# Kernel tuning notes

Measured on AMD Instinct MI355X. Metric: run time of the kernel, lower is better.

The kernel has to match this reference:

```python
import jax, jax.numpy as jnp
import numpy as np

SIZE, NC, BITS = 16, 3, 8
NV = NC * BITS * SIZE * SIZE  # 6144
NH = NV
N = 32
K_LS = 32   # fixed cap on T=0 local-search Gibbs sweeps (converged rows are fixed points)
K_CP = 16   # fixed cap on coupling MH iterations (converged rows masked out)


def float2bit(x, bits=BITS):
    # quantize [0,1) floats to `bits` binary planes, as in float2bit(...).flatten(1)
    q = jnp.clip(jnp.floor(x * (2 ** bits)), 0, 2 ** bits - 1).astype(jnp.int32)
    shifts = jnp.arange(bits, dtype=jnp.int32)
    b = (q[..., None] >> shifts) & 1  # [N,nc,H,W,bits]
    return b.astype(jnp.float32)


def energy(params, v, h0, h1):
    W0, W1, b0, b1, b2 = params
    e = -jnp.sum(v * b0, axis=1)
    e = e - jnp.sum(h0 * (v @ W0.T + b1), axis=1)
    e = e - jnp.sum(h1 * (h0 @ W1.T + b2), axis=1)
    return e


def _samp(logits, r, T):
    if T == 0:
        return (logits >= 0).astype(jnp.float32)
    return (r < jax.nn.sigmoid(logits / T)).astype(jnp.float32)


def gibbs_step(params, v, h0, h1, even, fix_v, T, key):
    W0, W1, b0, b1, b2 = params
    if T == 0:
        rv = rh0 = rh1 = None
    else:
        kv, k0, k1 = jax.random.split(key, 3)
        rv = jax.random.uniform(kv, v.shape)
        rh0 = jax.random.uniform(k0, h0.shape)
        rh1 = jax.random.uniform(k1, h1.shape)
    # 'even' sweep order: v -> odd h layers -> even h layers
    v_e = v if fix_v else _samp(h0 @ W0 + b0, rv, T)
    h1_e = _samp(h0 @ W1.T + b2, rh1, T)
    h0_e = _samp(v_e @ W0.T + b1 + h1_e @ W1, rh0, T)
    # 'odd' sweep order: even h layers -> v -> odd h layers
    h0_o = _samp(v @ W0.T + b1 + h1 @ W1, rh0, T)
    v_o = v if fix_v else _samp(h0_o @ W0 + b0, rv, T)
    h1_o = _samp(h0_o @ W1.T + b2, rh1, T)
    m = even[:, None]
    return (jnp.where(m, v_e, v_o), jnp.where(m, h0_e, h0_o), jnp.where(m, h1_e, h1_o))


def local_search(params, v, h0, h1, fix_v, key):
    # T=0 deterministic descent with a fixed per-row even/odd split (rand_u drawn once);
    # converged rows are fixed points of the map, so running a fixed K_LS sweeps over the
    # full batch is equivalent to the torch masked while-loop (up to the iteration cap).
    even = jax.random.uniform(key, (v.shape[0],)) < 0.5
    def body(i, s):
        return gibbs_step(params, s[0], s[1], s[2], even, fix_v, 0, None)
    return jax.lax.fori_loop(0, K_LS, body, (v, h0, h1))


def mh_step(params, v, h0, h1, fix_v, key):
    kv, k0, k1, ku = jax.random.split(key, 4)
    v_p = v if fix_v else (jax.random.uniform(kv, v.shape) < 0.5).astype(jnp.float32)
    h0_p = (jax.random.uniform(k0, h0.shape) < 0.5).astype(jnp.float32)
    h1_p = (jax.random.uniform(k1, h1.shape) < 0.5).astype(jnp.float32)
    log_ratio = energy(params, v, h0, h1) - energy(params, v_p, h0_p, h1_p)
    acc = jax.random.uniform(ku, (v.shape[0],)) < jnp.exp(jnp.minimum(log_ratio, 0.0))
    a = acc[:, None]
    return (v if fix_v else jnp.where(a, v_p, v), jnp.where(a, h0_p, h0), jnp.where(a, h1_p, h1))


def _conv_mask(v_new, h0_new, h1_new, v, h0, h1, fix_v):
    c = jnp.ones(v.shape[0], bool) if fix_v else jnp.all(v_new == v, axis=1)
    return c & jnp.all(h0_new == h0, axis=1) & jnp.all(h1_new == h1, axis=1)


def coupling(params, v, h0, h1, fix_v, key):
    k0, key = jax.random.split(key)
    v1, h01, h11 = mh_step(params, v, h0, h1, fix_v, k0)
    e = energy(params, v1, h01, h11)
    conv = _conv_mask(v1, h01, h11, v, h0, h1, fix_v)
    def body(state, k):
        v, h0, h1, e, conv = state
        v2, h02, h12 = mh_step(params, v, h0, h1, fix_v, k)
        de = energy(params, v2, h02, h12) - energy(params, v, h0, h1)
        m = ~conv
        e = e + jnp.where(m, de, 0.0)
        conv2 = _conv_mask(v2, h02, h12, v, h0, h1, fix_v)
        mm = m[:, None]
        v = jnp.where(mm, v2, v)
        h0 = jnp.where(mm, h02, h0)
        h1 = jnp.where(mm, h12, h1)
        return (v, h0, h1, e, conv | conv2), None
    keys = jax.random.split(key, K_CP)
    (v, h0, h1, e, conv), _ = jax.lax.scan(body, (v1, h01, h11, e, conv), keys)
    return e, v, h0, h1


def _dbm_loss(v_img, W0, W1, b0, b1, b2):
    params = (W0, W1, b0, b1, b2)
    n = v_img.shape[0]
    ks = jax.random.split(jax.random.key(42), 13)
    v = float2bit(v_img).reshape(n, -1)
    # positive phase (visibles clamped, fix_v=True)
    h0 = (jax.random.uniform(ks[0], (n, NH)) < 0.5).astype(jnp.float32)
    h1 = (jax.random.uniform(ks[1], (n, NH)) < 0.5).astype(jnp.float32)
    v, h0, h1 = local_search(params, v, h0, h1, True, ks[2])
    even = jax.random.uniform(ks[3], (n,)) < 0.5
    v, h0, h1 = gibbs_step(params, v, h0, h1, even, True, 1, ks[4])
    e_pos, v, h0, h1 = coupling(params, v, h0, h1, True, ks[5])
    # negative phase (free-running)
    v = (jax.random.uniform(ks[6], v.shape) < 0.5).astype(jnp.float32)
    h0 = (jax.random.uniform(ks[7], (n, NH)) < 0.5).astype(jnp.float32)
    h1 = (jax.random.uniform(ks[8], (n, NH)) < 0.5).astype(jnp.float32)
    v, h0, h1 = local_search(params, v, h0, h1, False, ks[9])
    even = jax.random.uniform(ks[10], (n,)) < 0.5
    v, h0, h1 = gibbs_step(params, v, h0, h1, even, False, 1, ks[11])
    e_neg, v, h0, h1 = coupling(params, v, h0, h1, False, ks[12])
    return e_pos - e_neg  # [N]


def setup_inputs() -> dict:
    key = jax.random.key(0)
    kv, kw0, kw1 = jax.random.split(key, 3)
    v = jax.random.uniform(kv, (N, NC, SIZE, SIZE), dtype=jnp.float32)
    # orthogonal-like scale (unit-norm rows): entries ~ 1/sqrt(fan_in)
    W0 = jax.random.normal(kw0, (NH, NV), dtype=jnp.float32) / np.sqrt(NV)
    W1 = jax.random.normal(kw1, (NH, NH), dtype=jnp.float32) / np.sqrt(NH)
    b0 = jnp.zeros((NV,), jnp.float32)
    b1 = jnp.zeros((NH,), jnp.float32)
    b2 = jnp.zeros((NH,), jnp.float32)
    return {"v": v, "W0": W0, "W1": W1, "b0": b0, "b1": b1, "b2": b2}


def reference(v, W0, W1, b0, b1, b2):
    return _dbm_loss(v, W0, W1, b0, b1, b2)
```

## Files before the change

kernel.cpp:

```cpp
#include <hip/hip_runtime.h>
#include <cstdint>
#include <math.h>

typedef unsigned int u32;
typedef unsigned long long u64;
typedef double d4 __attribute__((ext_vector_type(4)));

#define TF_PARTITIONABLE 1

#define NU 6144
#define NB 32
#define NTOT (NU * NB)
#define NWORD 96
#define NCH 16
#define CHK 384
#define NT_TILES 12
#define HALF_BIG 98304u
#define HALF_SMALL 16u

struct Key { u32 a, b; };
struct UVec { float u[NB]; };

__host__ __device__ __forceinline__ void tf2x32(u32 k0, u32 k1, u32 x0, u32 x1, u32& o0, u32& o1) {
  const u32 k2 = k0 ^ k1 ^ 0x1BD11BDAu;
#define TFR(r) { x0 += x1; x1 = (x1 << r) | (x1 >> (32 - r)); x1 ^= x0; }
  x0 += k0; x1 += k1;
  TFR(13) TFR(15) TFR(26) TFR(6)  x0 += k1; x1 += k2 + 1u;
  TFR(17) TFR(29) TFR(16) TFR(24) x0 += k2; x1 += k0 + 2u;
  TFR(13) TFR(15) TFR(26) TFR(6)  x0 += k0; x1 += k1 + 3u;
  TFR(17) TFR(29) TFR(16) TFR(24) x0 += k1; x1 += k2 + 4u;
  TFR(13) TFR(15) TFR(26) TFR(6)  x0 += k2; x1 += k0 + 5u;
#undef TFR
  o0 = x0; o1 = x1;
}

__host__ __device__ __forceinline__ u32 rbits(u32 k0, u32 k1, u32 t, u32 half) {
#if TF_PARTITIONABLE
  (void)half;
  u32 a, b; tf2x32(k0, k1, 0u, t, a, b); return a ^ b;
#else
  u32 a, b;
  if (t < half) { tf2x32(k0, k1, t, half + t, a, b); return a; }
  tf2x32(k0, k1, t - half, t, a, b); return b;
#endif
}

__host__ __device__ __forceinline__ float u01f(u32 bits) {
  union { u32 u; float f; } c; c.u = (bits >> 9) | 0x3f800000u;
  return c.f - 1.0f;
}

__device__ __forceinline__ double pav(int probe, int l) {
  return probe ? (double)(((l * 13 + 5) & 63) + 1) : (double)(l + 1);
}
__device__ __forceinline__ double pbv(int probe, int l) {
  return probe ? (double)(((l * 11 + 2) & 63) + 1) : (double)(((l * 7 + 3) & 63) + 1);
}

__global__ __launch_bounds__(64) void k_calib(int* __restrict__ tbl) {
  int L = threadIdx.x;
  d4 z = {0.0, 0.0, 0.0, 0.0};
  d4 o0 = __builtin_amdgcn_mfma_f64_16x16x4f64(pav(0, L), pbv(0, L), z, 0, 0, 0);
  d4 o1 = __builtin_amdgcn_mfma_f64_16x16x4f64(pav(1, L), pbv(1, L), z, 0, 0, 0);
  int q = L >> 4, m16 = L & 15;
  int best = -1;
  for (int combo = 0; combo < 16; ++combo) {
    int fa = combo & 1, fb = (combo >> 1) & 1, fd = combo >> 2;
    int ok = 1;
    for (int probe = 0; probe < 2; ++probe) {
#pragma unroll
      for (int r = 0; r < 4; ++r) {
        int i, j;
        if (fd == 0)      { j = m16; i = 4 * q + r; }
        else if (fd == 1) { j = m16; i = q + 4 * r; }
        else if (fd == 2) { i = m16; j = 4 * q + r; }
        else              { i = m16; j = q + 4 * r; }
        double pred = 0.0;
#pragma unroll
        for (int k = 0; k < 4; ++k) {
          int la = fa ? (i * 4 + k) : (k * 16 + i);
          int lb = fb ? (j * 4 + k) : (k * 16 + j);
          pred += pav(probe, la) * pbv(probe, lb);
        }
        double obs = probe ? (r == 0 ? o1[0] : r == 1 ? o1[1] : r == 2 ? o1[2] : o1[3])
                           : (r == 0 ? o0[0] : r == 1 ? o0[1] : r == 2 ? o0[2] : o0[3]);
        if (pred != obs) ok = 0;
      }
    }
    if (__all(ok) && best < 0) best = combo;
  }
  int mA = 0, kA = 0, nB = 0, kB = 0, b0_ = 0, bs = 0, j0 = 0, js = 0, okf = 0;
  if (best >= 0) {
    int fa = best & 1, fb = (best >> 1) & 1, fd = best >> 2;
    if (fa) { mA = L >> 2; kA = L & 3; } else { mA = m16; kA = q; }
    if (fb) { nB = L >> 2; kB = L & 3; } else { nB = m16; kB = q; }
    if (fd == 0)      { j0 = m16; js = 0; b0_ = 4 * q; bs = 1; }
    else if (fd == 1) { j0 = m16; js = 0; b0_ = q; bs = 4; }
    else if (fd == 2) { b0_ = m16; bs = 0; j0 = 4 * q; js = 1; }
    else              { b0_ = m16; bs = 0; j0 = q; js = 4; }
    okf = 1;
  }
  int* p = tbl + L * 16;
  p[0] = mA; p[1] = kA; p[2] = nB; p[3] = kB;
  p[4] = b0_; p[5] = bs; p[6] = j0; p[7] = js; p[8] = okf;
}

__global__ void k_init(u32* __restrict__ flag, u32* __restrict__ chg) { *flag = 0u; *chg = 0u; }

__global__ void k_conv(u32* __restrict__ flag, u32* __restrict__ chg) {
  if (*flag == 0u && *chg == 0u) *flag = 1u;
  *chg = 0u;
}

__global__ void k_allconv(const u32* __restrict__ conv, u32* __restrict__ skipc) {
  if (*skipc) return;
  u32 all = 1u;
  for (int b = 0; b < NB; ++b) all &= conv[b];
  if (all) *skipc = 1u;
}

__global__ __launch_bounds__(256) void k_pos_v(const float* __restrict__ vin, u64* __restrict__ pk) {
  int tid = blockIdx.x * 256 + threadIdx.x;
  int b = tid / 768, p = tid % 768;
  float x = vin[tid];
  int q = (int)floorf(x * 256.0f);
  q = q < 0 ? 0 : (q > 255 ? 255 : q);
  ((unsigned char*)pk)[b * 768 + p] = (unsigned char)q;
}

__global__ __launch_bounds__(256) void k_bern(u32 k0, u32 k1, u64* __restrict__ pk) {
  int tid = blockIdx.x * 256 + threadIdx.x;
  bool s = u01f(rbits(k0, k1, (u32)tid, HALF_BIG)) < 0.5f;
  u64 m = __ballot(s);
  if ((threadIdx.x & 63) == 0) pk[tid >> 6] = m;
}

__global__ __launch_bounds__(256) void k_bern3(u32 has_v, u32 va, u32 vb, u32 ha0, u32 hb0,
                                               u32 ha1, u32 hb1,
                                               u64* __restrict__ pkv, u64* __restrict__ pkh0,
                                               u64* __restrict__ pkh1, const u32* __restrict__ skip) {
  if (skip && *skip) return;
  int tid = blockIdx.x * 256 + threadIdx.x;
  int lane0 = (threadIdx.x & 63) == 0;
  if (has_v) {
    bool s = u01f(rbits(va, vb, (u32)tid, HALF_BIG)) < 0.5f;
    u64 m = __ballot(s);
    if (lane0) pkv[tid >> 6] = m;
  }
  { bool s = u01f(rbits(ha0, hb0, (u32)tid, HALF_BIG)) < 0.5f;
    u64 m = __ballot(s);
    if (lane0) pkh0[tid >> 6] = m; }
  { bool s = u01f(rbits(ha1, hb1, (u32)tid, HALF_BIG)) < 0.5f;
    u64 m = __ballot(s);
    if (lane0) pkh1[tid >> 6] = m; }
}

__device__ __forceinline__ bool samp_dec(float f, int t1, u32 k0, u32 k1, u32 tid) {
  if (t1) {
    double u = (double)u01f(rbits(k0, k1, tid, HALF_BIG));
    return u < 1.0 / (1.0 + exp(-(double)f));
  }
  return f >= 0.0f;
}

__global__ __launch_bounds__(256) void k_samp(const float* __restrict__ fE, const float* __restrict__ fO,
                                              u32 even, int t1, u32 k0, u32 k1,
                                              u64* __restrict__ pk,
                                              const u32* __restrict__ skip, u32* __restrict__ chg) {
  if (skip && *skip) return;
  int tid = blockIdx.x * 256 + threadIdx.x;
  int b = tid / NU;
  float f = ((even >> b) & 1u) ? fE[tid] : fO[tid];
  bool s = samp_dec(f, t1, k0, k1, (u32)tid);
  u64 m = __ballot(s);
  if ((threadIdx.x & 63) == 0) {
    int widx = tid >> 6;
    if (chg) { u64 old = pk[widx]; if (old != m) *chg = 1u; }
    pk[widx] = m;
  }
}

__global__ __launch_bounds__(256) void k_gemm_n(const float* __restrict__ W, const u64* __restrict__ pkx,
                                                double* __restrict__ part, const u32* __restrict__ skip,
                                                const int* __restrict__ tbl) {
  if (skip && *skip) return;
  __shared__ double smem_d[2560];
  int jt = blockIdx.x % 96, c = blockIdx.x / 96;
  int wid = threadIdx.x >> 6, lane = threadIdx.x & 63;
  int kbase = c * CHK;
  int jn0 = jt * 64;
  const int* tp = tbl + lane * 16;
  int okf = tp[8];
  if (okf) {
    float* lw = (float*)smem_d;
    int mA = tp[0], kA = tp[1], nB = tp[2], kB = tp[3];
    int bD0 = tp[4], bDs = tp[5], jD0 = tp[6], jDs = tp[7];
    int t256 = threadIdx.x;
    d4 acc0 = {0.0, 0.0, 0.0, 0.0};
    d4 acc1 = {0.0, 0.0, 0.0, 0.0};
#pragma unroll
    for (int r = 0; r < 2; ++r) {
      int idx = r * 256 + t256, kk = idx >> 4, qq = idx & 15;
      float4 w4 = *(const float4*)(W + (size_t)(kbase + kk) * NU + jn0 + 4 * qq);
      float* d = &lw[kk * 80 + 4 * qq];
      d[0] = w4.x; d[1] = w4.y; d[2] = w4.z; d[3] = w4.w;
    }
    __syncthreads();
    const u64* pxr0 = pkx + (size_t)mA * NWORD + (kbase >> 6);
    const u64* pxr1 = pkx + (size_t)(mA + 16) * NWORD + (kbase >> 6);
    int buf = 0;
    for (int t = 0; t < NT_TILES; ++t) {
      float4 w0p, w1p;
      bool pf = (t + 1) < NT_TILES;
      if (pf) {
        int k0n = kbase + (t + 1) * 32;
        { int idx = t256,       kk = idx >> 4, qq = idx & 15;
          w0p = *(const float4*)(W + (size_t)(k0n + kk) * NU + jn0 + 4 * qq); }
        { int idx = 256 + t256, kk = idx >> 4, qq = idx & 15;
          w1p = *(const float4*)(W + (size_t)(k0n + kk) * NU + jn0 + 4 * qq); }
      }
      u64 ww0 = pxr0[t >> 1], ww1 = pxr1[t >> 1];
      u32 sh = ((u32)(t & 1) << 5) + (u32)kA;
      u32 bb0 = (u32)(ww0 >> sh), bb1 = (u32)(ww1 >> sh);
      const float* lwp = &lw[(buf * 32 + kB) * 80 + wid * 16 + nB];
#pragma unroll
      for (int u = 0; u < 8; ++u) {
        double a0 = (double)((bb0 >> (4 * u)) & 1u);
        double a1 = (double)((bb1 >> (4 * u)) & 1u);
        double wv = (double)lwp[320 * u];
        acc0 = __builtin_amdgcn_mfma_f64_16x16x4f64(a0, wv, acc0, 0, 0, 0);
        acc1 = __builtin_amdgcn_mfma_f64_16x16x4f64(a1, wv, acc1, 0, 0, 0);
      }
      if (pf) {
        int nb = buf ^ 1;
        { int idx = t256,       kk = idx >> 4, qq = idx & 15;
          float* d = &lw[(nb * 32 + kk) * 80 + 4 * qq];
          d[0] = w0p.x; d[1] = w0p.y; d[2] = w0p.z; d[3] = w0p.w; }
        { int idx = 256 + t256, kk = idx >> 4, qq = idx & 15;
          float* d = &lw[(nb * 32 + kk) * 80 + 4 * qq];
          d[0] = w1p.x; d[1] = w1p.y; d[2] = w1p.z; d[3] = w1p.w; }
      }
      __syncthreads();
      buf ^= 1;
    }
    int jn = jn0 + wid * 16;
    double* pp = part + (size_t)c * NTOT + jn;
#pragma unroll
    for (int r = 0; r < 4; ++r) {
      int bi = bD0 + bDs * r, jj = jD0 + jDs * r;
      pp[(size_t)bi * NU + jj] = acc0[r];
      pp[(size_t)(bi + 16) * NU + jj] = acc1[r];
    }
  } else {
    double* red = smem_d;
    int j = jn0 + lane;
    int i0 = kbase + wid * (CHK / 4);
    const float* wp = W + (size_t)i0 * NU + j;
    double acc[32];
#pragma unroll
    for (int b = 0; b < 32; ++b) acc[b] = 0.0;
    for (int i = 0; i < CHK / 4; ++i) {
      double w = (double)wp[(size_t)i * NU];
      int k = i0 + i;
#pragma unroll
      for (int b = 0; b < 32; ++b) {
        double xb = (double)((pkx[(size_t)b * NWORD + (k >> 6)] >> (k & 63)) & 1ull);
        acc[b] = fma(xb, w, acc[b]);
      }
    }
    for (int w = 1; w < 4; ++w) {
      if (wid == w) {
#pragma unroll
        for (int b = 0; b < 32; ++b) red[b * 64 + lane] = acc[b];
      }
      __syncthreads();
      if (wid == 0) {
#pragma unroll
        for (int b = 0; b < 32; ++b) acc[b] += red[b * 64 + lane];
      }
      __syncthreads();
    }
    if (wid == 0) {
      double* pp = part + (size_t)c * NTOT + j;
#pragma unroll
      for (int b = 0; b < 32; ++b) pp[(size_t)b * NU] = acc[b];
    }
  }
}

__global__ __launch_bounds__(256) void k_gemm_t(const float* __restrict__ W, const u64* __restrict__ pkx,
                                                double* __restrict__ part, const u32* __restrict__ skip,
                                                const int* __restrict__ tbl) {
  if (skip && *skip) return;
  __shared__ double smem_d[2176];
  int jt = blockIdx.x % 96, c = blockIdx.x / 96;
  int wid = threadIdx.x >> 6, lane = threadIdx.x & 63;
  int kbase = c * CHK;
  int jn0 = jt * 64;
  const int* tp = tbl + lane * 16;
  int okf = tp[8];
  if (okf) {
    float* lw = (float*)smem_d;
    int mA = tp[0], kA = tp[1], nB = tp[2], kB = tp[3];
    int bD0 = tp[4], bDs = tp[5], jD0 = tp[6], jDs = tp[7];
    int t256 = threadIdx.x;
    d4 acc0 = {0.0, 0.0, 0.0, 0.0};
    d4 acc1 = {0.0, 0.0, 0.0, 0.0};
#pragma unroll
    for (int r = 0; r < 2; ++r) {
      int idx = r * 256 + t256, jj = idx >> 3, kq = idx & 7;
      float4 w4 = *(const float4*)(W + (size_t)(jn0 + jj) * NU + kbase + 4 * kq);
      float* d = &lw[jj * 34 + 4 * kq];
      d[0] = w4.x; d[1] = w4.y; d[2] = w4.z; d[3] = w4.w;
    }
    __syncthreads();
    const u64* pxr0 = pkx + (size_t)mA * NWORD + (kbase >> 6);
    const u64* pxr1 = pkx + (size_t)(mA + 16) * NWORD + (kbase >> 6);
    int buf = 0;
    for (int t = 0; t < NT_TILES; ++t) {
      float4 w0p, w1p;
      bool pf = (t + 1) < NT_TILES;
      if (pf) {
        int k0n = kbase + (t + 1) * 32;
        { int idx = t256,       jj = idx >> 3, kq = idx & 7;
          w0p = *(const float4*)(W + (size_t)(jn0 + jj) * NU + k0n + 4 * kq); }
        { int idx = 256 + t256, jj = idx >> 3, kq = idx & 7;
          w1p = *(const float4*)(W + (size_t)(jn0 + jj) * NU + k0n + 4 * kq); }
      }
      u64 ww0 = pxr0[t >> 1], ww1 = pxr1[t >> 1];
      u32 sh = ((u32)(t & 1) << 5) + (u32)kA;
      u32 bb0 = (u32)(ww0 >> sh), bb1 = (u32)(ww1 >> sh);
      const float* lwp = &lw[(buf * 64 + wid * 16 + nB) * 34 + kB];
#pragma unroll
      for (int u = 0; u < 8; ++u) {
        double a0 = (double)((bb0 >> (4 * u)) & 1u);
        double a1 = (double)((bb1 >> (4 * u)) & 1u);
        double wv = (double)lwp[4 * u];
        acc0 = __builtin_amdgcn_mfma_f64_16x16x4f64(a0, wv, acc0, 0, 0, 0);
        acc1 = __builtin_amdgcn_mfma_f64_16x16x4f64(a1, wv, acc1, 0, 0, 0);
      }
      if (pf) {
        int nb = buf ^ 1;
        { int idx = t256,       jj = idx >> 3, kq = idx & 7;
          float* d = &lw[(nb * 64 + jj) * 34 + 4 * kq];
          d[0] = w0p.x; d[1] = w0p.y; d[2] = w0p.z; d[3] = w0p.w; }
        { int idx = 256 + t256, jj = idx >> 3, kq = idx & 7;
          float* d = &lw[(nb * 64 + jj) * 34 + 4 * kq];
          d[0] = w1p.x; d[1] = w1p.y; d[2] = w1p.z; d[3] = w1p.w; }
      }
      __syncthreads();
      buf ^= 1;
    }
    int jn = jn0 + wid * 16;
    double* pp = part + (size_t)c * NTOT + jn;
#pragma unroll
    for (int r = 0; r < 4; ++r) {
      int bi = bD0 + bDs * r, jj = jD0 + jDs * r;
      pp[(size_t)bi * NU + jj] = acc0[r];
      pp[(size_t)(bi + 16) * NU + jj] = acc1[r];
    }
  } else {
    float* lwf = (float*)smem_d;
    double* red = smem_d;
    int qf = threadIdx.x & 7, af = threadIdx.x >> 3;
    double acc[32];
#pragma unroll
    for (int b = 0; b < 32; ++b) acc[b] = 0.0;
    for (int s = 0; s < NT_TILES; ++s) {
      int ib = kbase + s * 32;
#pragma unroll
      for (int pass = 0; pass < 2; ++pass) {
        int r = pass * 32 + af;
        float4 w4 = *(const float4*)(W + (size_t)(jn0 + r) * NU + ib + qf * 4);
        lwf[(qf * 4 + 0) * 65 + r] = w4.x;
        lwf[(qf * 4 + 1) * 65 + r] = w4.y;
        lwf[(qf * 4 + 2) * 65 + r] = w4.z;
        lwf[(qf * 4 + 3) * 65 + r] = w4.w;
      }
      __syncthreads();
      int iw = wid * 8;
      for (int ii = 0; ii < 8; ++ii) {
        double w = (double)lwf[(iw + ii) * 65 + lane];
        int k = ib + iw + ii;
#pragma unroll
        for (int b = 0; b < 32; ++b) {
          double xb = (double)((pkx[(size_t)b * NWORD + (k >> 6)] >> (k & 63)) & 1ull);
          acc[b] = fma(xb, w, acc[b]);
        }
      }
      __syncthreads();
    }
    for (int w = 1; w < 4; ++w) {
      if (wid == w) {
#pragma unroll
        for (int b = 0; b < 32; ++b) red[b * 64 + lane] = acc[b];
      }
      __syncthreads();
      if (wid == 0) {
#pragma unroll
        for (int b = 0; b < 32; ++b) acc[b] += red[b * 64 + lane];
      }
      __syncthreads();
    }
    if (wid == 0) {
      double* pp = part + (size_t)c * NTOT + jn0 + lane;
#pragma unroll
      for (int b = 0; b < 32; ++b) pp[(size_t)b * NU] = acc[b];
    }
  }
}

__global__ __launch_bounds__(256) void k_reduce(const double* __restrict__ part, const float* __restrict__ bias,
                                                const float* __restrict__ src, float* __restrict__ out,
                                                const u32* __restrict__ skip) {
  if (skip && *skip) return;
  int tid = blockIdx.x * 256 + threadIdx.x;
  int j = tid % NU;
  double s = src ? (double)src[tid] : 0.0;
  if (bias) s += (double)bias[j];
#pragma unroll
  for (int c = 0; c < NCH; ++c) s += part[(size_t)c * NTOT + tid];
  out[tid] = (float)s;
}

__global__ __launch_bounds__(256) void k_redsamp(const double* __restrict__ part, const float* __restrict__ bias,
                                                 const float* __restrict__ src, float* __restrict__ out,
                                                 int t1, u32 k0, u32 k1,
                                                 u64* __restrict__ pk,
                                                 const u32* __restrict__ skip, u32 wmask,
                                                 u32* __restrict__ chg) {
  if (skip && *skip) return;
  int tid = blockIdx.x * 256 + threadIdx.x;
  int j = tid % NU, b = tid / NU;
  double s = src ? (double)src[tid] : 0.0;
  if (bias) s += (double)bias[j];
#pragma unroll
  for (int c = 0; c < NCH; ++c) s += part[(size_t)c * NTOT + tid];
  float f = (float)s;
  if (out) out[tid] = f;
  bool wr = (wmask >> b) & 1u;
  bool smp = samp_dec(f, t1, k0, k1, (u32)tid);
  u64 m = __ballot(smp);
  if (((threadIdx.x & 63) == 0) && wr) {
    int widx = tid >> 6;
    if (chg) { u64 old = pk[widx]; if (old != m) *chg = 1u; }
    pk[widx] = m;
  }
  (void)j;
}

__global__ __launch_bounds__(256) void k_energy(const u64* __restrict__ pkv, const u64* __restrict__ pkh0,
                                                const u64* __restrict__ pkh1, const float* __restrict__ f1,
                                                const float* __restrict__ f2, const float* __restrict__ b0,
                                                float* __restrict__ eout, const u32* __restrict__ skip) {
  if (skip && *skip) return;
  __shared__ double red[256];
  int b = blockIdx.x, t = threadIdx.x;
  double s = 0.0;
  for (int j = t; j < NU; j += 256) {
    int w = j >> 6, bit = j & 63;
    if ((pkv [b * NWORD + w] >> bit) & 1ull) s += (double)b0[j];
    if ((pkh0[b * NWORD + w] >> bit) & 1ull) s += (double)f1[(size_t)b * NU + j];
    if ((pkh1[b * NWORD + w] >> bit) & 1ull) s += (double)f2[(size_t)b * NU + j];
  }
  red[t] = s; __syncthreads();
  for (int off = 128; off > 0; off >>= 1) { if (t < off) red[t] += red[t + off]; __syncthreads(); }
  if (t == 0) eout[b] = (float)(-red[0]);
}

__global__ __launch_bounds__(64) void k_accept(float* __restrict__ ecur, const float* __restrict__ eprop,
                                               float* __restrict__ erun, u32* __restrict__ conv,
                                               u32* __restrict__ accf,
                                               const u64* __restrict__ pv, const u64* __restrict__ pcv,
                                               const u64* __restrict__ ph0, const u64* __restrict__ pch0,
                                               const u64* __restrict__ ph1, const u64* __restrict__ pch1,
                                               UVec uv, int first, const u32* __restrict__ skip) {
  if (skip && *skip) return;
  int b = blockIdx.x, t = threadIdx.x;
  u64 diff = 0ull;
  for (int w = t; w < NWORD; w += 64) {
    size_t o = (size_t)b * NWORD + w;
    if (pv) diff |= pv[o] ^ pcv[o];
    diff |= ph0[o] ^ pch0[o];
    diff |= ph1[o] ^ pch1[o];
  }
  int neq = __any(diff != 0ull);
  if (t == 0) {
    float ec = ecur[b], ep = eprop[b];
    bool acc = (double)uv.u[b] < exp(fmin((double)ec - (double)ep, 0.0));
    bool m = first ? true : (conv[b] == 0u);
    bool upd = m && acc;
    if (first) erun[b] = acc ? ep : ec;
    else if (upd) erun[b] += (ep - ec);
    if (upd) ecur[b] = ep;
    u32 c2 = acc ? (neq ? 0u : 1u) : 1u;
    conv[b] = first ? c2 : (conv[b] | c2);
    accf[b] = upd ? 1u : 0u;
  }
}

__global__ __launch_bounds__(256) void k_merge_pk(const u32* __restrict__ accf,
                                                  const u64* __restrict__ pa, u64* __restrict__ ca,
                                                  const u64* __restrict__ pb, u64* __restrict__ cb,
                                                  const u64* __restrict__ pc, u64* __restrict__ cc,
                                                  const u32* __restrict__ skip) {
  if (skip && *skip) return;
  int w = blockIdx.x * 256 + threadIdx.x;
  if (w >= NB * NWORD) return;
  int b = w / NWORD;
  if (accf[b]) {
    ca[w] = pa[w];
    cb[w] = pb[w];
    if (pc) cc[w] = pc[w];
  }
}

__global__ void k_final(const float* __restrict__ ep, const float* __restrict__ en, float* __restrict__ out) {
  int b = threadIdx.x;
  if (b < NB) out[b] = ep[b] - en[b];
}

static void split_keys(Key k, int n, Key* out) {
#if TF_PARTITIONABLE
  for (int i = 0; i < n; ++i) { u32 a, b; tf2x32(k.a, k.b, 0u, (u32)i, a, b); out[i].a = a; out[i].b = b; }
#else
  u32 flat[64];
  for (int i = 0; i < n; ++i) { u32 a, b; tf2x32(k.a, k.b, (u32)i, (u32)(n + i), a, b); flat[i] = a; flat[n + i] = b; }
  for (int i = 0; i < n; ++i) { out[i].a = flat[2 * i]; out[i].b = flat[2 * i + 1]; }
#endif
}
static u32 mask32(Key k) {
  u32 m = 0;
  for (int b = 0; b < NB; ++b)
    if (u01f(rbits(k.a, k.b, (u32)b, HALF_SMALL)) < 0.5f) m |= (1u << b);
  return m;
}

extern "C" void kernel_launch(void* const* d_in, const int* in_sizes, int n_in,
                              void* d_out, int out_size, void* d_ws, size_t ws_size,
                              hipStream_t stream) {
  const float* vin = (const float*)d_in[0];
  const float* W0  = (const float*)d_in[1];
  const float* W1  = (const float*)d_in[2];
  const float* b0  = (const float*)d_in[3];
  const float* b1  = (const float*)d_in[4];
  const float* b2  = (const float*)d_in[5];
  float* outp = (float*)d_out;

  char* ws = (char*)d_ws;
  size_t off = 0;
  auto alloc = [&](size_t bytes) -> void* {
    void* p = ws + off; off += (bytes + 255) & ~(size_t)255; return p;
  };
  enum { SV = 0, SH0, SH1, SVE, SH1E, SH0O, SVP, SH0P, SH1P, NS };
  enum { IV = 0, IA, IB, IC, ID, IE, IF2, NF };
  u64* PK[NS]; float* F[NF];
  for (int f = 0; f < NF; ++f) F[f] = (float*)alloc((size_t)NTOT * 4);
  double* PART = (double*)alloc((size_t)NCH * NTOT * 8);
  for (int s = 0; s < NS; ++s) PK[s] = (u64*)alloc((size_t)NB * NWORD * 8);
  int*   TBL    = (int*)alloc(64 * 16 * 4);
  float* E_CUR  = (float*)alloc(256);
  float* E_PROP = (float*)alloc(256);
  float* E_POS  = (float*)alloc(256);
  float* E_NEG  = (float*)alloc(256);
  u32*   ACC    = (u32*)alloc(256);
  u32*   CONV   = (u32*)alloc(256);
  u32*   FLAG   = (u32*)alloc(256);
  u32*   CHG    = (u32*)alloc(256);
  u32*   SKIPC  = (u32*)alloc(256);
  u32*   DUMMY  = (u32*)alloc(256);
  if (off > ws_size) return;

  Key root{0u, 42u};
  Key ks[13]; split_keys(root, 13, ks);
  const Key KZ{0u, 0u};

  k_calib<<<dim3(1), dim3(64), 0, stream>>>(TBL);

  auto GEMM_T = [&](const float* Wm, int xs, const u32* skip) {
    k_gemm_t<<<dim3(96 * NCH), dim3(256), 0, stream>>>(Wm, PK[xs], PART, skip, TBL);
  };
  auto GEMM_N = [&](const float* Wm, int xs, const u32* skip) {
    k_gemm_n<<<dim3(96 * NCH), dim3(256), 0, stream>>>(Wm, PK[xs], PART, skip, TBL);
  };
  auto RED = [&](const float* bias, const float* src, float* dst, const u32* skip) {
    k_reduce<<<dim3(768), dim3(256), 0, stream>>>(PART, bias, src, dst, skip);
  };
  auto REDS = [&](const float* bias, const float* src, float* dst, int t1, Key k, int sdst,
                  const u32* skip, u32 wm, u32* chg) {
    k_redsamp<<<dim3(768), dim3(256), 0, stream>>>(PART, bias, src, dst, t1, k.a, k.b,
                                                   PK[sdst], skip, wm, chg);
  };
  auto GT = [&](const float* Wm, int xs, const float* bias, const float* src, float* dst, const u32* skip) {
    GEMM_T(Wm, xs, skip); RED(bias, src, dst, skip);
  };
  auto GN = [&](const float* Wm, int xs, const float* bias, const float* src, float* dst, const u32* skip) {
    GEMM_N(Wm, xs, skip); RED(bias, src, dst, skip);
  };
  auto GTS = [&](const float* Wm, int xs, const float* bias, const float* src, float* dst,
                 int t1, Key k, int sdst, const u32* skip) {
    GEMM_T(Wm, xs, skip); REDS(bias, src, dst, t1, k, sdst, skip, ~0u, nullptr);
  };
  auto GNS = [&](const float* Wm, int xs, const float* bias, const float* src, float* dst,
                 int t1, Key k, int sdst, const u32* skip) {
    GEMM_N(Wm, xs, skip); REDS(bias, src, dst, t1, k, sdst, skip, ~0u, nullptr);
  };
  auto SAMP = [&](const float* fE, const float* fO, u32 even, int t1, Key k, int dst,
                  const u32* skip, u32* chg) {
    k_samp<<<dim3(768), dim3(256), 0, stream>>>(fE, fO, even, t1, k.a, k.b, PK[dst], skip, chg);
  };
  auto BERN = [&](Key k, int dst) {
    k_bern<<<dim3(768), dim3(256), 0, stream>>>(k.a, k.b, PK[dst]);
  };
  auto ENERGY = [&](int sv, int sh0, int sh1, const float* f1, const float* f2, float* eo, const u32* skip) {
    k_energy<<<dim3(32), dim3(256), 0, stream>>>(PK[sv], PK[sh0], PK[sh1], f1, f2, b0, eo, skip);
  };

  auto ls_fixv = [&](u32 evm) {
    auto X = [&](u32 wm) {
      GEMM_T(W1, SH0, FLAG);
      REDS(b2, nullptr, nullptr, 0, KZ, SH1, FLAG, wm, CHG);
    };
    auto Y = [&]() {
      GEMM_N(W1, SH1, FLAG);
      REDS(nullptr, F[IV], nullptr, 0, KZ, SH0, FLAG, ~0u, CHG);
    };
    k_init<<<dim3(1), dim3(1), 0, stream>>>(FLAG, CHG);
    X(evm);
    for (int i = 0; i < 31; ++i) {
      Y(); X(~0u);
      k_conv<<<dim3(1), dim3(1), 0, stream>>>(FLAG, CHG);
    }
    Y(); X(~evm);
  };
  auto ls_free = [&](u32 evm) {
    auto X = [&](u32 wm) {
      GEMM_N(W0, SH0, FLAG);
      REDS(b0, nullptr, nullptr, 0, KZ, SV, FLAG, wm, CHG);
      GEMM_T(W1, SH0, FLAG);
      REDS(b2, nullptr, nullptr, 0, KZ, SH1, FLAG, wm, CHG);
    };
    auto Y = [&]() {
      GT(W0, SV, b1, nullptr, F[IC], FLAG);
      GEMM_N(W1, SH1, FLAG);
      REDS(nullptr, F[IC], nullptr, 0, KZ, SH0, FLAG, ~0u, CHG);
    };
    k_init<<<dim3(1), dim3(1), 0, stream>>>(FLAG, CHG);
    X(evm);
    for (int i = 0; i < 31; ++i) {
      Y(); X(~0u);
      k_conv<<<dim3(1), dim3(1), 0, stream>>>(FLAG, CHG);
    }
    Y(); X(~evm);
  };

  auto gibbs_fixv = [&](u32 even, Key kh0, Key kh1) {
    GTS(W1, SH0, b2, nullptr, F[IA], 1, kh1, SH1E, nullptr);
    GN(W1, SH1E, nullptr, F[IV], F[IB], nullptr);
    GNS(W1, SH1, nullptr, F[IV], F[IC], 1, kh0, SH0O, nullptr);
    GT(W1, SH0O, b2, nullptr, F[ID], nullptr);
    SAMP(F[IB], F[IC], even, 1, kh0, SH0, nullptr, nullptr);
    SAMP(F[IA], F[ID], even, 1, kh1, SH1, nullptr, nullptr);
  };
  auto gibbs_free = [&](u32 even, Key kv, Key kh0, Key kh1) {
    GNS(W0, SH0, b0, nullptr, F[IE], 1, kv, SVE, nullptr);
    GTS(W1, SH0, b2, nullptr, F[IA], 1, kh1, SH1E, nullptr);
    GT(W0, SVE, b1, nullptr, F[IB], nullptr);
    GN(W1, SH1E, nullptr, F[IB], F[IB], nullptr);
    GT(W0, SV, b1, nullptr, F[IC], nullptr);
    GNS(W1, SH1, nullptr, F[IC], F[IC], 1, kh0, SH0O, nullptr);
    GN(W0, SH0O, b0, nullptr, F[IF2], nullptr);
    GT(W1, SH0O, b2, nullptr, F[ID], nullptr);
    SAMP(F[IE], F[IF2], even, 1, kv, SV, nullptr, nullptr);
    SAMP(F[IB], F[IC], even, 1, kh0, SH0, nullptr, nullptr);
    SAMP(F[IA], F[ID], even, 1, kh1, SH1, nullptr, nullptr);
  };

  auto coupling = [&](bool fixv, Key ck, float* erun) {
    Key top[2]; split_keys(ck, 2, top);
    Key cks[17]; cks[0] = top[0];
    { Key rest[16]; split_keys(top[1], 16, rest); for (int i = 0; i < 16; ++i) cks[i + 1] = rest[i]; }
    k_init<<<dim3(1), dim3(1), 0, stream>>>(SKIPC, DUMMY);
    for (int it = 0; it < 17; ++it) {
      const u32* sk = (it == 0) ? nullptr : SKIPC;
      Key sub[4]; split_keys(cks[it], 4, sub);
      UVec uv;
      for (int b = 0; b < NB; ++b) uv.u[b] = u01f(rbits(sub[3].a, sub[3].b, (u32)b, HALF_SMALL));
      k_bern3<<<dim3(768), dim3(256), 0, stream>>>(fixv ? 0u : 1u,
          sub[0].a, sub[0].b, sub[1].a, sub[1].b, sub[2].a, sub[2].b,
          PK[SVP], PK[SH0P], PK[SH1P], sk);
      const float* f1;
      if (fixv) f1 = F[IV];
      else { GT(W0, SVP, b1, nullptr, F[IC], sk); f1 = F[IC]; }
      GT(W1, SH0P, b2, nullptr, F[ID], sk);
      ENERGY(fixv ? SV : SVP, SH0P, SH1P, f1, F[ID], E_PROP, sk);
      k_accept<<<dim3(32), dim3(64), 0, stream>>>(E_CUR, E_PROP, erun, CONV, ACC,
          fixv ? nullptr : PK[SVP], fixv ? nullptr : PK[SV],
          PK[SH0P], PK[SH0], PK[SH1P], PK[SH1], uv, it == 0 ? 1 : 0, sk);
      k_merge_pk<<<dim3(12), dim3(256), 0, stream>>>(ACC, PK[SH0P], PK[SH0], PK[SH1P], PK[SH1],
          fixv ? nullptr : PK[SVP], fixv ? nullptr : PK[SV], sk);
      k_allconv<<<dim3(1), dim3(1), 0, stream>>>(CONV, SKIPC);
    }
  };

  k_pos_v<<<dim3(96), dim3(256), 0, stream>>>(vin, PK[SV]);
  BERN(ks[0], SH0);
  BERN(ks[1], SH1);
  GT(W0, SV, b1, nullptr, F[IV], nullptr);
  u32 ev_ls_pos = mask32(ks[2]);
  ls_fixv(ev_ls_pos);
  u32 ev2_pos = mask32(ks[3]);
  Key g4[3]; split_keys(ks[4], 3, g4);
  gibbs_fixv(ev2_pos, g4[1], g4[2]);
  GT(W1, SH0, b2, nullptr, F[ID], nullptr);
  ENERGY(SV, SH0, SH1, F[IV], F[ID], E_CUR, nullptr);
  coupling(true, ks[5], E_POS);

  BERN(ks[6], SV);
  BERN(ks[7], SH0);
  BERN(ks[8], SH1);
  u32 ev_ls_neg = mask32(ks[9]);
  ls_free(ev_ls_neg);
  u32 ev2_neg = mask32(ks[10]);
  Key g11[3]; split_keys(ks[11], 3, g11);
  gibbs_free(ev2_neg, g11[0], g11[1], g11[2]);
  GT(W0, SV, b1, nullptr, F[IB], nullptr);
  GT(W1, SH0, b2, nullptr, F[IA], nullptr);
  ENERGY(SV, SH0, SH1, F[IB], F[IA], E_CUR, nullptr);
  coupling(false, ks[12], E_NEG);

  k_final<<<dim3(1), dim3(64), 0, stream>>>(E_POS, E_NEG, outp);
}
```

Before: 13.50 ms.

## Batch independent GEMMs into paired launches and detect period-2 cycles in local search

Independent matrix-vector products that consume the same or unrelated inputs now run in one paired GEMM launch with a doubled grid, and their reductions and sampling are fused into one paired reduce-sample kernel. The K split changes from 16 chunks of 384 to 12 chunks of 512. Local-search convergence no longer uses per-word change flags with atomics. Instead it snapshots state into two alternating slots and stops early when a state repeats two sweeps later, restoring the correct parity with a fixup kernel. This cuts launch count and partial-sum traffic and may skip more sweeps, at the cost of extra snapshot copies and more complex convergence logic.

```diff
diff --git a/kernel.cpp b/kernel.cpp
--- a/kernel.cpp
+++ b/kernel.cpp
@@ -12,14 +12,18 @@
 #define NB 32
 #define NTOT (NU * NB)
 #define NWORD 96
-#define NCH 16
-#define CHK 384
-#define NT_TILES 12
+#define SW (NB * NWORD)
+#define NCH 12
+#define CHK 512
+#define NT_TILES 16
+#define GGRID (96 * NCH)
 #define HALF_BIG 98304u
 #define HALF_SMALL 16u
 
 struct Key { u32 a, b; };
 struct UVec { float u[NB]; };
+struct RS { const double* part; const float* bias; const float* src; float* out;
+            int t1; u32 k0, k1; u64* pk; u32 wm; };
 
 __host__ __device__ __forceinline__ void tf2x32(u32 k0, u32 k1, u32 x0, u32 x1, u32& o0, u32& o1) {
   const u32 k2 = k0 ^ k1 ^ 0x1BD11BDAu;
@@ -105,18 +109,49 @@
   p[4] = b0_; p[5] = bs; p[6] = j0; p[7] = js; p[8] = okf;
 }
 
-__global__ void k_init(u32* __restrict__ flag, u32* __restrict__ chg) { *flag = 0u; *chg = 0u; }
-
-__global__ void k_conv(u32* __restrict__ flag, u32* __restrict__ chg) {
-  if (*flag == 0u && *chg == 0u) *flag = 1u;
-  *chg = 0u;
-}
+__global__ void k_init(u32* __restrict__ a, u32* __restrict__ b) { *a = 0u; *b = 0u; }
 
 __global__ void k_allconv(const u32* __restrict__ conv, u32* __restrict__ skipc) {
   if (*skipc) return;
   u32 all = 1u;
   for (int b = 0; b < NB; ++b) all &= conv[b];
   if (all) *skipc = 1u;
+}
+
+__global__ __launch_bounds__(256) void k_cyc(const u64* __restrict__ s0, const u64* __restrict__ s1,
+                                             const u64* __restrict__ s2, u64* __restrict__ save,
+                                             int slot, int docmp, int rem_odd, int prev_slot,
+                                             u32* __restrict__ flag, u32* __restrict__ fix) {
+  if (*flag) return;
+  __shared__ u32 neq_sh;
+  if (threadIdx.x == 0) neq_sh = 0u;
+  __syncthreads();
+  u64* sp = save + (size_t)slot * (3 * SW);
+  u32 neq = 0;
+  for (int w = threadIdx.x; w < SW; w += 256) {
+    u64 a0 = s0[w]; if (a0 != sp[w]) neq = 1; sp[w] = a0;
+    u64 a1 = s1[w]; if (a1 != sp[SW + w]) neq = 1; sp[SW + w] = a1;
+    if (s2) { u64 a2 = s2[w]; if (a2 != sp[2 * SW + w]) neq = 1; sp[2 * SW + w] = a2; }
+  }
+  if (neq) neq_sh = 1u;
+  __syncthreads();
+  if (threadIdx.x == 0 && docmp && neq_sh == 0u) {
+    *flag = 1u;
+    *fix = rem_odd ? (1u + (u32)prev_slot) : 0u;
+  }
+}
+
+__global__ __launch_bounds__(256) void k_fixup(u64* __restrict__ s0, u64* __restrict__ s1,
+                                               u64* __restrict__ s2, const u64* __restrict__ save,
+                                               const u32* __restrict__ flag, const u32* __restrict__ fix) {
+  if (!*flag || !*fix) return;
+  const u64* sp = save + (size_t)(*fix - 1u) * (3 * SW);
+  int w = blockIdx.x * 256 + threadIdx.x;
+  if (w < SW) {
+    s0[w] = sp[w];
+    s1[w] = sp[SW + w];
+    if (s2) s2[w] = sp[2 * SW + w];
+  }
 }
 
 __global__ __launch_bounds__(256) void k_pos_v(const float* __restrict__ vin, u64* __restrict__ pk) {
@@ -164,28 +199,19 @@
 }
 
 __global__ __launch_bounds__(256) void k_samp(const float* __restrict__ fE, const float* __restrict__ fO,
-                                              u32 even, int t1, u32 k0, u32 k1,
-                                              u64* __restrict__ pk,
-                                              const u32* __restrict__ skip, u32* __restrict__ chg) {
-  if (skip && *skip) return;
+                                              u32 even, int t1, u32 k0, u32 k1, u64* __restrict__ pk) {
   int tid = blockIdx.x * 256 + threadIdx.x;
   int b = tid / NU;
   float f = ((even >> b) & 1u) ? fE[tid] : fO[tid];
   bool s = samp_dec(f, t1, k0, k1, (u32)tid);
   u64 m = __ballot(s);
-  if ((threadIdx.x & 63) == 0) {
-    int widx = tid >> 6;
-    if (chg) { u64 old = pk[widx]; if (old != m) *chg = 1u; }
-    pk[widx] = m;
-  }
-}
-
-__global__ __launch_bounds__(256) void k_gemm_n(const float* __restrict__ W, const u64* __restrict__ pkx,
-                                                double* __restrict__ part, const u32* __restrict__ skip,
-                                                const int* __restrict__ tbl) {
-  if (skip && *skip) return;
-  __shared__ double smem_d[2560];
-  int jt = blockIdx.x % 96, c = blockIdx.x / 96;
+  if ((threadIdx.x & 63) == 0) pk[tid >> 6] = m;
+}
+
+__device__ __forceinline__ void gemm_n_body(int bid, const float* __restrict__ W,
+                                            const u64* __restrict__ pkx, double* __restrict__ part,
+                                            const int* __restrict__ tbl, double* smem_d) {
+  int jt = bid % 96, c = bid / 96;
   int wid = threadIdx.x >> 6, lane = threadIdx.x & 63;
   int kbase = c * CHK;
   int jn0 = jt * 64;
@@ -288,12 +314,10 @@
   }
 }
 
-__global__ __launch_bounds__(256) void k_gemm_t(const float* __restrict__ W, const u64* __restrict__ pkx,
-                                                double* __restrict__ part, const u32* __restrict__ skip,
-                                                const int* __restrict__ tbl) {
-  if (skip && *skip) return;
-  __shared__ double smem_d[2176];
-  int jt = blockIdx.x % 96, c = blockIdx.x / 96;
+__device__ __forceinline__ void gemm_t_body(int bid, const float* __restrict__ W,
+                                            const u64* __restrict__ pkx, double* __restrict__ part,
+                                            const int* __restrict__ tbl, double* smem_d) {
+  int jt = bid % 96, c = bid / 96;
   int wid = threadIdx.x >> 6, lane = threadIdx.x & 63;
   int kbase = c * CHK;
   int jn0 = jt * 64;
@@ -410,43 +434,57 @@
   }
 }
 
-__global__ __launch_bounds__(256) void k_reduce(const double* __restrict__ part, const float* __restrict__ bias,
-                                                const float* __restrict__ src, float* __restrict__ out,
-                                                const u32* __restrict__ skip) {
+__global__ __launch_bounds__(256) void k_gemm2(int ta, const float* __restrict__ Wa,
+                                               const u64* __restrict__ pka, double* __restrict__ partA,
+                                               int tb, const float* __restrict__ Wb,
+                                               const u64* __restrict__ pkb, double* __restrict__ partB,
+                                               const u32* __restrict__ skip, const int* __restrict__ tbl) {
+  if (skip && *skip) return;
+  __shared__ double smem[2560];
+  int h = (blockIdx.x >= (u32)GGRID) ? 1 : 0;
+  int bid = blockIdx.x - h * GGRID;
+  int tt = h ? tb : ta;
+  const float* W = h ? Wb : Wa;
+  const u64* pk = h ? pkb : pka;
+  double* part = h ? partB : partA;
+  if (tt) gemm_t_body(bid, W, pk, part, tbl, smem);
+  else    gemm_n_body(bid, W, pk, part, tbl, smem);
+}
+
+__global__ __launch_bounds__(256) void k_rs2(RS A, RS B, const u32* __restrict__ skip) {
+  if (skip && *skip) return;
+  int h = (blockIdx.x >= 768u) ? 1 : 0;
+  RS& r = h ? B : A;
+  int tid = (blockIdx.x - h * 768) * 256 + threadIdx.x;
+  int j = tid % NU, b = tid / NU;
+  double s = r.src ? (double)r.src[tid] : 0.0;
+  if (r.bias) s += (double)r.bias[j];
+#pragma unroll
+  for (int c = 0; c < NCH; ++c) s += r.part[(size_t)c * NTOT + tid];
+  float f = (float)s;
+  if (r.out) r.out[tid] = f;
+  bool smp = samp_dec(f, r.t1, r.k0, r.k1, (u32)tid);
+  u64 m = __ballot(smp);
+  if (((threadIdx.x & 63) == 0) && r.pk && ((r.wm >> b) & 1u)) r.pk[tid >> 6] = m;
+}
+
+__global__ __launch_bounds__(256) void k_rs_s2(const double* __restrict__ partA, const float* __restrict__ bias1,
+                                               const double* __restrict__ partB, u64* __restrict__ pk,
+                                               const u32* __restrict__ skip) {
   if (skip && *skip) return;
   int tid = blockIdx.x * 256 + threadIdx.x;
   int j = tid % NU;
-  double s = src ? (double)src[tid] : 0.0;
-  if (bias) s += (double)bias[j];
-#pragma unroll
-  for (int c = 0; c < NCH; ++c) s += part[(size_t)c * NTOT + tid];
-  out[tid] = (float)s;
-}
-
-__global__ __launch_bounds__(256) void k_redsamp(const double* __restrict__ part, const float* __restrict__ bias,
-                                                 const float* __restrict__ src, float* __restrict__ out,
-                                                 int t1, u32 k0, u32 k1,
-                                                 u64* __restrict__ pk,
-                                                 const u32* __restrict__ skip, u32 wmask,
-                                                 u32* __restrict__ chg) {
-  if (skip && *skip) return;
-  int tid = blockIdx.x * 256 + threadIdx.x;
-  int j = tid % NU, b = tid / NU;
-  double s = src ? (double)src[tid] : 0.0;
-  if (bias) s += (double)bias[j];
-#pragma unroll
-  for (int c = 0; c < NCH; ++c) s += part[(size_t)c * NTOT + tid];
+  double sA = (double)bias1[j];
+#pragma unroll
+  for (int c = 0; c < NCH; ++c) sA += partA[(size_t)c * NTOT + tid];
+  float t = (float)sA;
+  double s = (double)t;
+#pragma unroll
+  for (int c = 0; c < NCH; ++c) s += partB[(size_t)c * NTOT + tid];
   float f = (float)s;
-  if (out) out[tid] = f;
-  bool wr = (wmask >> b) & 1u;
-  bool smp = samp_dec(f, t1, k0, k1, (u32)tid);
+  bool smp = (f >= 0.0f);
   u64 m = __ballot(smp);
-  if (((threadIdx.x & 63) == 0) && wr) {
-    int widx = tid >> 6;
-    if (chg) { u64 old = pk[widx]; if (old != m) *chg = 1u; }
-    pk[widx] = m;
-  }
-  (void)j;
+  if ((threadIdx.x & 63) == 0) pk[tid >> 6] = m;
 }
 
 __global__ __launch_bounds__(256) void k_energy(const u64* __restrict__ pkv, const u64* __restrict__ pkh0,
@@ -556,8 +594,10 @@
   enum { IV = 0, IA, IB, IC, ID, IE, IF2, NF };
   u64* PK[NS]; float* F[NF];
   for (int f = 0; f < NF; ++f) F[f] = (float*)alloc((size_t)NTOT * 4);
-  double* PART = (double*)alloc((size_t)NCH * NTOT * 8);
+  double* PARTA = (double*)alloc((size_t)2 * NCH * NTOT * 8);
+  double* PARTB = PARTA + (size_t)NCH * NTOT;
   for (int s = 0; s < NS; ++s) PK[s] = (u64*)alloc((size_t)NB * NWORD * 8);
+  u64*   SAVE   = (u64*)alloc((size_t)2 * 3 * SW * 8);
   int*   TBL    = (int*)alloc(64 * 16 * 4);
   float* E_CUR  = (float*)alloc(256);
   float* E_PROP = (float*)alloc(256);
@@ -566,7 +606,7 @@
   u32*   ACC    = (u32*)alloc(256);
   u32*   CONV   = (u32*)alloc(256);
   u32*   FLAG   = (u32*)alloc(256);
-  u32*   CHG    = (u32*)alloc(256);
+  u32*   FIX    = (u32*)alloc(256);
   u32*   SKIPC  = (u32*)alloc(256);
   u32*   DUMMY  = (u32*)alloc(256);
   if (off > ws_size) return;
@@ -577,37 +617,27 @@
 
   k_calib<<<dim3(1), dim3(64), 0, stream>>>(TBL);
 
-  auto GEMM_T = [&](const float* Wm, int xs, const u32* skip) {
-    k_gemm_t<<<dim3(96 * NCH), dim3(256), 0, stream>>>(Wm, PK[xs], PART, skip, TBL);
-  };
-  auto GEMM_N = [&](const float* Wm, int xs, const u32* skip) {
-    k_gemm_n<<<dim3(96 * NCH), dim3(256), 0, stream>>>(Wm, PK[xs], PART, skip, TBL);
-  };
-  auto RED = [&](const float* bias, const float* src, float* dst, const u32* skip) {
-    k_reduce<<<dim3(768), dim3(256), 0, stream>>>(PART, bias, src, dst, skip);
-  };
-  auto REDS = [&](const float* bias, const float* src, float* dst, int t1, Key k, int sdst,
-                  const u32* skip, u32 wm, u32* chg) {
-    k_redsamp<<<dim3(768), dim3(256), 0, stream>>>(PART, bias, src, dst, t1, k.a, k.b,
-                                                   PK[sdst], skip, wm, chg);
-  };
-  auto GT = [&](const float* Wm, int xs, const float* bias, const float* src, float* dst, const u32* skip) {
-    GEMM_T(Wm, xs, skip); RED(bias, src, dst, skip);
-  };
-  auto GN = [&](const float* Wm, int xs, const float* bias, const float* src, float* dst, const u32* skip) {
-    GEMM_N(Wm, xs, skip); RED(bias, src, dst, skip);
-  };
-  auto GTS = [&](const float* Wm, int xs, const float* bias, const float* src, float* dst,
-                 int t1, Key k, int sdst, const u32* skip) {
-    GEMM_T(Wm, xs, skip); REDS(bias, src, dst, t1, k, sdst, skip, ~0u, nullptr);
-  };
-  auto GNS = [&](const float* Wm, int xs, const float* bias, const float* src, float* dst,
-                 int t1, Key k, int sdst, const u32* skip) {
-    GEMM_N(Wm, xs, skip); REDS(bias, src, dst, t1, k, sdst, skip, ~0u, nullptr);
-  };
-  auto SAMP = [&](const float* fE, const float* fO, u32 even, int t1, Key k, int dst,
-                  const u32* skip, u32* chg) {
-    k_samp<<<dim3(768), dim3(256), 0, stream>>>(fE, fO, even, t1, k.a, k.b, PK[dst], skip, chg);
+  auto mkrs = [&](const double* part, const float* bias, const float* src, float* out,
+                  int t1, Key k, u64* pk, u32 wm) {
+    RS r; r.part = part; r.bias = bias; r.src = src; r.out = out;
+    r.t1 = t1; r.k0 = k.a; r.k1 = k.b; r.pk = pk; r.wm = wm; return r;
+  };
+  auto GEMM1 = [&](int tt, const float* Wm, int xs, const u32* skip) {
+    k_gemm2<<<dim3(GGRID), dim3(256), 0, stream>>>(tt, Wm, PK[xs], PARTA,
+                                                   0, Wm, PK[xs], PARTB, skip, TBL);
+  };
+  auto GEMM2 = [&](int ta, const float* Wa, int xa, int tb, const float* Wb, int xb, const u32* skip) {
+    k_gemm2<<<dim3(2 * GGRID), dim3(256), 0, stream>>>(ta, Wa, PK[xa], PARTA,
+                                                       tb, Wb, PK[xb], PARTB, skip, TBL);
+  };
+  auto RS1 = [&](RS a, const u32* skip) {
+    k_rs2<<<dim3(768), dim3(256), 0, stream>>>(a, a, skip);
+  };
+  auto RS2 = [&](RS a, RS b, const u32* skip) {
+    k_rs2<<<dim3(1536), dim3(256), 0, stream>>>(a, b, skip);
+  };
+  auto SAMP = [&](const float* fE, const float* fO, u32 even, int t1, Key k, int dst) {
+    k_samp<<<dim3(768), dim3(256), 0, stream>>>(fE, fO, even, t1, k.a, k.b, PK[dst]);
   };
   auto BERN = [&](Key k, int dst) {
     k_bern<<<dim3(768), dim3(256), 0, stream>>>(k.a, k.b, PK[dst]);
@@ -617,63 +647,72 @@
   };
 
   auto ls_fixv = [&](u32 evm) {
-    auto X = [&](u32 wm) {
-      GEMM_T(W1, SH0, FLAG);
-      REDS(b2, nullptr, nullptr, 0, KZ, SH1, FLAG, wm, CHG);
+    auto X = [&](u32 wm, const u32* skip) {
+      GEMM1(1, W1, SH0, skip);
+      RS1(mkrs(PARTA, b2, nullptr, nullptr, 0, KZ, PK[SH1], wm), skip);
     };
-    auto Y = [&]() {
-      GEMM_N(W1, SH1, FLAG);
-      REDS(nullptr, F[IV], nullptr, 0, KZ, SH0, FLAG, ~0u, CHG);
+    auto Y = [&](const u32* skip) {
+      GEMM1(0, W1, SH1, skip);
+      RS1(mkrs(PARTA, nullptr, F[IV], nullptr, 0, KZ, PK[SH0], ~0u), skip);
     };
-    k_init<<<dim3(1), dim3(1), 0, stream>>>(FLAG, CHG);
-    X(evm);
-    for (int i = 0; i < 31; ++i) {
-      Y(); X(~0u);
-      k_conv<<<dim3(1), dim3(1), 0, stream>>>(FLAG, CHG);
-    }
-    Y(); X(~evm);
+    k_init<<<dim3(1), dim3(1), 0, stream>>>(FLAG, FIX);
+    X(evm, nullptr);
+    for (int i = 1; i <= 31; ++i) {
+      Y(FLAG); X(~0u, FLAG);
+      k_cyc<<<dim3(1), dim3(256), 0, stream>>>(PK[SH0], PK[SH1], nullptr, SAVE,
+          i & 1, (i >= 3) ? 1 : 0, (31 - i) & 1, (i - 1) & 1, FLAG, FIX);
+    }
+    k_fixup<<<dim3(12), dim3(256), 0, stream>>>(PK[SH0], PK[SH1], nullptr, SAVE, FLAG, FIX);
+    Y(nullptr); X(~evm, nullptr);
   };
   auto ls_free = [&](u32 evm) {
-    auto X = [&](u32 wm) {
-      GEMM_N(W0, SH0, FLAG);
-      REDS(b0, nullptr, nullptr, 0, KZ, SV, FLAG, wm, CHG);
-      GEMM_T(W1, SH0, FLAG);
-      REDS(b2, nullptr, nullptr, 0, KZ, SH1, FLAG, wm, CHG);
+    auto X = [&](u32 wm, const u32* skip) {
+      GEMM2(0, W0, SH0, 1, W1, SH0, skip);
+      RS2(mkrs(PARTA, b0, nullptr, nullptr, 0, KZ, PK[SV], wm),
+          mkrs(PARTB, b2, nullptr, nullptr, 0, KZ, PK[SH1], wm), skip);
     };
-    auto Y = [&]() {
-      GT(W0, SV, b1, nullptr, F[IC], FLAG);
-      GEMM_N(W1, SH1, FLAG);
-      REDS(nullptr, F[IC], nullptr, 0, KZ, SH0, FLAG, ~0u, CHG);
+    auto Y = [&](const u32* skip) {
+      GEMM2(1, W0, SV, 0, W1, SH1, skip);
+      k_rs_s2<<<dim3(768), dim3(256), 0, stream>>>(PARTA, b1, PARTB, PK[SH0], skip);
     };
-    k_init<<<dim3(1), dim3(1), 0, stream>>>(FLAG, CHG);
-    X(evm);
-    for (int i = 0; i < 31; ++i) {
-      Y(); X(~0u);
-      k_conv<<<dim3(1), dim3(1), 0, stream>>>(FLAG, CHG);
-    }
-    Y(); X(~evm);
+    k_init<<<dim3(1), dim3(1), 0, stream>>>(FLAG, FIX);
+    X(evm, nullptr);
+    for (int i = 1; i <= 31; ++i) {
+      Y(FLAG); X(~0u, FLAG);
+      k_cyc<<<dim3(1), dim3(256), 0, stream>>>(PK[SV], PK[SH0], PK[SH1], SAVE,
+          i & 1, (i >= 3) ? 1 : 0, (31 - i) & 1, (i - 1) & 1, FLAG, FIX);
+    }
+    k_fixup<<<dim3(12), dim3(256), 0, stream>>>(PK[SV], PK[SH0], PK[SH1], SAVE, FLAG, FIX);
+    Y(nullptr); X(~evm, nullptr);
   };
 
   auto gibbs_fixv = [&](u32 even, Key kh0, Key kh1) {
-    GTS(W1, SH0, b2, nullptr, F[IA], 1, kh1, SH1E, nullptr);
-    GN(W1, SH1E, nullptr, F[IV], F[IB], nullptr);
-    GNS(W1, SH1, nullptr, F[IV], F[IC], 1, kh0, SH0O, nullptr);
-    GT(W1, SH0O, b2, nullptr, F[ID], nullptr);
-    SAMP(F[IB], F[IC], even, 1, kh0, SH0, nullptr, nullptr);
-    SAMP(F[IA], F[ID], even, 1, kh1, SH1, nullptr, nullptr);
+    GEMM1(1, W1, SH0, nullptr);
+    RS1(mkrs(PARTA, b2, nullptr, F[IA], 1, kh1, PK[SH1E], ~0u), nullptr);
+    GEMM2(0, W1, SH1E, 0, W1, SH1, nullptr);
+    RS2(mkrs(PARTA, nullptr, F[IV], F[IB], 0, KZ, nullptr, 0),
+        mkrs(PARTB, nullptr, F[IV], F[IC], 1, kh0, PK[SH0O], ~0u), nullptr);
+    GEMM1(1, W1, SH0O, nullptr);
+    RS1(mkrs(PARTA, b2, nullptr, F[ID], 0, KZ, nullptr, 0), nullptr);
+    SAMP(F[IB], F[IC], even, 1, kh0, SH0);
+    SAMP(F[IA], F[ID], even, 1, kh1, SH1);
   };
   auto gibbs_free = [&](u32 even, Key kv, Key kh0, Key kh1) {
-    GNS(W0, SH0, b0, nullptr, F[IE], 1, kv, SVE, nullptr);
-    GTS(W1, SH0, b2, nullptr, F[IA], 1, kh1, SH1E, nullptr);
-    GT(W0, SVE, b1, nullptr, F[IB], nullptr);
-    GN(W1, SH1E, nullptr, F[IB], F[IB], nullptr);
-    GT(W0, SV, b1, nullptr, F[IC], nullptr);
-    GNS(W1, SH1, nullptr, F[IC], F[IC], 1, kh0, SH0O, nullptr);
-    GN(W0, SH0O, b0, nullptr, F[IF2], nullptr);
-    GT(W1, SH0O, b2, nullptr, F[ID], nullptr);
-    SAMP(F[IE], F[IF2], even, 1, kv, SV, nullptr, nullptr);
-    SAMP(F[IB], F[IC], even, 1, kh0, SH0, nullptr, nullptr);
-    SAMP(F[IA], F[ID], even, 1, kh1, SH1, nullptr, nullptr);
+    GEMM2(0, W0, SH0, 1, W1, SH0, nullptr);
+    RS2(mkrs(PARTA, b0, nullptr, F[IE], 1, kv, PK[SVE], ~0u),
+        mkrs(PARTB, b2, nullptr, F[IA], 1, kh1, PK[SH1E], ~0u), nullptr);
+    GEMM2(1, W0, SVE, 1, W0, SV, nullptr);
+    RS2(mkrs(PARTA, b1, nullptr, F[IB], 0, KZ, nullptr, 0),
+        mkrs(PARTB, b1, nullptr, F[IC], 0, KZ, nullptr, 0), nullptr);
+    GEMM2(0, W1, SH1E, 0, W1, SH1, nullptr);
+    RS2(mkrs(PARTA, nullptr, F[IB], F[IB], 0, KZ, nullptr, 0),
+        mkrs(PARTB, nullptr, F[IC], F[IC], 1, kh0, PK[SH0O], ~0u), nullptr);
+    GEMM2(0, W0, SH0O, 1, W1, SH0O, nullptr);
+    RS2(mkrs(PARTA, b0, nullptr, F[IF2], 0, KZ, nullptr, 0),
+        mkrs(PARTB, b2, nullptr, F[ID], 0, KZ, nullptr, 0), nullptr);
+    SAMP(F[IE], F[IF2], even, 1, kv, SV);
+    SAMP(F[IB], F[IC], even, 1, kh0, SH0);
+    SAMP(F[IA], F[ID], even, 1, kh1, SH1);
   };
 
   auto coupling = [&](bool fixv, Key ck, float* erun) {
@@ -690,9 +729,16 @@
           sub[0].a, sub[0].b, sub[1].a, sub[1].b, sub[2].a, sub[2].b,
           PK[SVP], PK[SH0P], PK[SH1P], sk);
       const float* f1;
-      if (fixv) f1 = F[IV];
-      else { GT(W0, SVP, b1, nullptr, F[IC], sk); f1 = F[IC]; }
-      GT(W1, SH0P, b2, nullptr, F[ID], sk);
+      if (fixv) {
+        GEMM1(1, W1, SH0P, sk);
+        RS1(mkrs(PARTA, b2, nullptr, F[ID], 0, KZ, nullptr, 0), sk);
+        f1 = F[IV];
+      } else {
+        GEMM2(1, W0, SVP, 1, W1, SH0P, sk);
+        RS2(mkrs(PARTA, b1, nullptr, F[IC], 0, KZ, nullptr, 0),
+            mkrs(PARTB, b2, nullptr, F[ID], 0, KZ, nullptr, 0), sk);
+        f1 = F[IC];
+      }
       ENERGY(fixv ? SV : SVP, SH0P, SH1P, f1, F[ID], E_PROP, sk);
       k_accept<<<dim3(32), dim3(64), 0, stream>>>(E_CUR, E_PROP, erun, CONV, ACC,
           fixv ? nullptr : PK[SVP], fixv ? nullptr : PK[SV],
@@ -706,13 +752,15 @@
   k_pos_v<<<dim3(96), dim3(256), 0, stream>>>(vin, PK[SV]);
   BERN(ks[0], SH0);
   BERN(ks[1], SH1);
-  GT(W0, SV, b1, nullptr, F[IV], nullptr);
+  GEMM1(1, W0, SV, nullptr);
+  RS1(mkrs(PARTA, b1, nullptr, F[IV], 0, KZ, nullptr, 0), nullptr);
   u32 ev_ls_pos = mask32(ks[2]);
   ls_fixv(ev_ls_pos);
   u32 ev2_pos = mask32(ks[3]);
   Key g4[3]; split_keys(ks[4], 3, g4);
   gibbs_fixv(ev2_pos, g4[1], g4[2]);
-  GT(W1, SH0, b2, nullptr, F[ID], nullptr);
+  GEMM1(1, W1, SH0, nullptr);
+  RS1(mkrs(PARTA, b2, nullptr, F[ID], 0, KZ, nullptr, 0), nullptr);
   ENERGY(SV, SH0, SH1, F[IV], F[ID], E_CUR, nullptr);
   coupling(true, ks[5], E_POS);
 
@@ -724,8 +772,9 @@
   u32 ev2_neg = mask32(ks[10]);
   Key g11[3]; split_keys(ks[11], 3, g11);
   gibbs_free(ev2_neg, g11[0], g11[1], g11[2]);
-  GT(W0, SV, b1, nullptr, F[IB], nullptr);
-  GT(W1, SH0, b2, nullptr, F[IA], nullptr);
+  GEMM2(1, W0, SV, 1, W1, SH0, nullptr);
+  RS2(mkrs(PARTA, b1, nullptr, F[IB], 0, KZ, nullptr, 0),
+      mkrs(PARTB, b2, nullptr, F[IA], 0, KZ, nullptr, 0), nullptr);
   ENERGY(SV, SH0, SH1, F[IB], F[IA], E_CUR, nullptr);
   coupling(false, ks[12], E_NEG);
 
```

Result: slower. 18.00 ms (+33.4%).
